# Performance work log

Hardware: AMD Instinct MI355X
Metric: run time of the kernel (lower is better)

Reference implementation:

```python
import jax, jax.numpy as jnp
import numpy as np

SHIFT = 1  # fixed choice for the random +/-1 shift_direction in the torch module


def setup_inputs() -> dict:
    key = jax.random.key(0)
    kx, kw = jax.random.split(key)
    x = jax.random.normal(kx, (128, 128, 56, 56), dtype=jnp.float32)
    W = jax.random.normal(kw, (32, 3, 2, 3, 4), dtype=jnp.float32)
    return {"x": x, "W": W}


def reference(x, W):
    n = x.shape[0]
    # sum-pool over a factor-2 split of the channel dim: (n,128,56,56)->(n,64,56,56)
    t = x.reshape(n, 2, 64, 56, 56).sum(axis=1)
    # view channels as (32 groups, 2): (n,32,2,56,56)
    t = t.reshape(n, 32, 2, 56, 56)
    # first torch unfold == size-3 zero-padded window along the 32-group axis
    tp = jnp.pad(t, ((0, 0), (1, 1), (0, 0), (0, 0), (0, 0)))
    w1 = jnp.stack([tp[:, i:i + 32] for i in range(3)], axis=1)  # (n,3,32,2,56,56)
    # circular shift along the last spatial axis (torch.roll on dim 5)
    w1 = jnp.roll(w1, SHIFT, axis=5)
    # second torch unfold == size-3 zero-padded window along the rolled 56 axis
    wp = jnp.pad(w1, ((0, 0), (0, 0), (0, 0), (0, 0), (0, 0), (1, 1)))
    w2 = jnp.stack([wp[..., l:l + 56] for l in range(3)], axis=5)  # (n,3,32,2,56,3,56)
    # grouped local-conv contraction; axes: n,i=win1(3),j=32,m=2,p=56,l=win2(3),o=56; k=4
    out = jnp.einsum('nijmplo,jimlk->njpok', w2, W)  # (n,32,56,56,4)
    t5 = out.transpose(0, 2, 3, 1, 4).reshape(n, 56, 56, 128)
    t5 = jnp.roll(t5, SHIFT, axis=1)  # roll along first spatial axis
    return t5.transpose(0, 3, 1, 2)  # (n,128,56,56)
```

## Files before the change

### kernel.cpp

```cpp
#include <hip/hip_runtime.h>

#define TPB 512

__device__ __forceinline__ void compute28(const float4* __restrict__ sm4,
                                          const float wt[3][2][3],
                                          int j, int pl, int q0, int qb, int h,
                                          float acc[28]) {
#pragma unroll
    for (int u = 0; u < 28; ++u) acc[u] = 0.f;
#pragma unroll
    for (int i = 0; i < 3; ++i) {
        const int g = j + i - 1;
        if ((unsigned)g < 32u) {
#pragma unroll
            for (int m = 0; m < 2; ++m) {
                const float4* row4 = &sm4[((2 * g + m) * 2 + pl) * 15];
                float fe[32];
                { const float4 t = row4[q0]; fe[0] = t.x; fe[1] = t.y; fe[2] = t.z; fe[3] = t.w; }
#pragma unroll
                for (int q = 1; q < 8; ++q) {
                    const float4 t = row4[qb + q];
                    fe[4 * q + 0] = t.x; fe[4 * q + 1] = t.y;
                    fe[4 * q + 2] = t.z; fe[4 * q + 3] = t.w;
                }
                float va[30];
#pragma unroll
                for (int d = 0; d < 30; ++d) va[d] = fe[d + 2];
                va[0]  = h ? va[0] : 0.f;
                va[29] = h ? 0.f : va[29];
                const float w0 = wt[i][m][0];
                const float w1 = wt[i][m][1];
                const float w2 = wt[i][m][2];
#pragma unroll
                for (int u = 0; u < 28; ++u)
                    acc[u] += w0 * va[u] + w1 * va[u + 1] + w2 * va[u + 2];
            }
        }
    }
}

__device__ __forceinline__ void store2(float4* __restrict__ sm4, float4* __restrict__ o4,
                                       const float acc[28], int tid, int c, int h, int pl,
                                       int n, int p0) {
    const int chalf = c >> 6;
    const int cr = c & 63;
#pragma unroll
    for (int half = 0; half < 2; ++half) {
        __syncthreads();
        if (chalf == half) {
#pragma unroll
            for (int u4 = 0; u4 < 7; ++u4) {
                float4 v4;
                v4.x = acc[4 * u4 + 0];
                v4.y = acc[4 * u4 + 1];
                v4.z = acc[4 * u4 + 2];
                v4.w = acc[4 * u4 + 3];
                sm4[(cr + 64 * pl) * 15 + h * 7 + u4] = v4;
            }
        }
        __syncthreads();
#pragma unroll
        for (int it = 0; it < 4; ++it) {
            const int idx = tid + it * TPB;
            if (idx < 1792) {
                const int chp = idx / 14;
                const int v = idx - chp * 14;
                const int scr = chp & 63;
                const int spl = chp >> 6;
                o4[(size_t)(n * 128 + half * 64 + scr) * 784 + (size_t)(p0 + spl) * 14 + (size_t)v] =
                    sm4[chp * 15 + v];
            }
        }
    }
}

__global__ __launch_bounds__(TPB) void fused_shift_conv(const float* __restrict__ x,
                                                        const float* __restrict__ Wg,
                                                        float* __restrict__ out) {
    const int bid = blockIdx.x;
    const int ptile = bid % 28;
    const int n0 = (bid / 28) * 2;
    const int p0 = ptile * 2;
    const int P0 = (p0 + 55) % 56;
    const int P1 = p0;

    __shared__ float4 sm4[128 * 15];

    const int tid = threadIdx.x;
    const int pl = tid >> 8;
    const int t8 = tid & 255;
    const int h = t8 & 1;
    const int c = t8 >> 1;
    const int j = c >> 2;
    const int k = c & 3;
    const int q0 = h ? 6 : 13;
    const int qb = h ? 6 : -1;

    float wt[3][2][3];
#pragma unroll
    for (int i = 0; i < 3; ++i)
#pragma unroll
        for (int m = 0; m < 2; ++m)
#pragma unroll
            for (int l = 0; l < 3; ++l)
                wt[i][m][l] = Wg[(((j * 3 + i) * 2 + m) * 3 + l) * 4 + k];

    const float4* x4 = reinterpret_cast<const float4*>(x);

#pragma unroll
    for (int it = 0; it < 4; ++it) {
        const int idx = tid + it * TPB;
        if (idx < 1792) {
            const int S = idx / 14;
            const int v = idx - S * 14;
            const int r = S >> 1;
            const int q = S & 1;
            const int Pq = q ? P1 : P0;
            const size_t base = (size_t)(n0 * 128 + r) * 784 + (size_t)Pq * 14 + (size_t)v;
            const float4 a = x4[base];
            const float4 b = x4[base + (size_t)64 * 784];
            float4 s;
            s.x = a.x + b.x; s.y = a.y + b.y; s.z = a.z + b.z; s.w = a.w + b.w;
            sm4[S * 15 + v] = s;
        }
    }

    float4 pa[4], pb[4];
#pragma unroll
    for (int it = 0; it < 4; ++it) {
        const int idx = tid + it * TPB;
        if (idx < 1792) {
            const int S = idx / 14;
            const int v = idx - S * 14;
            const int r = S >> 1;
            const int q = S & 1;
            const int Pq = q ? P1 : P0;
            const size_t base = (size_t)((n0 + 1) * 128 + r) * 784 + (size_t)Pq * 14 + (size_t)v;
            pa[it] = x4[base];
            pb[it] = x4[base + (size_t)64 * 784];
        }
    }

    __syncthreads();

    float acc[28];
    compute28(sm4, wt, j, pl, q0, qb, h, acc);

#pragma unroll
    for (int it = 0; it < 4; ++it) {
        const int idx = tid + it * TPB;
        if (idx < 1792) {
            pa[it].x += pb[it].x; pa[it].y += pb[it].y;
            pa[it].z += pb[it].z; pa[it].w += pb[it].w;
        }
    }

    float4* o4 = reinterpret_cast<float4*>(out);
    store2(sm4, o4, acc, tid, c, h, pl, n0, p0);

    __syncthreads();

#pragma unroll
    for (int it = 0; it < 4; ++it) {
        const int idx = tid + it * TPB;
        if (idx < 1792) {
            const int S = idx / 14;
            const int v = idx - S * 14;
            sm4[S * 15 + v] = pa[it];
        }
    }
    __syncthreads();

    compute28(sm4, wt, j, pl, q0, qb, h, acc);
    store2(sm4, o4, acc, tid, c, h, pl, n0 + 1, p0);
}

extern "C" void kernel_launch(void* const* d_in, const int* in_sizes, int n_in,
                              void* d_out, int out_size, void* d_ws, size_t ws_size,
                              hipStream_t stream) {
    const float* x = (const float*)d_in[0];
    const float* W = (const float*)d_in[1];
    float* out = (float*)d_out;
    const int n = in_sizes[0] / (128 * 56 * 56);
    const int grid = (n / 2) * 28;
    fused_shift_conv<<<grid, TPB, 0, stream>>>(x, W, out);
}
```

Before: 106.7 us.

## Make blocks loop over row tiles with double-buffered LDS prefetch

Each block now handles one image and a quarter of the output rows, iterating over 7 row-pair tiles. The next tile's input is loaded into registers while the current tile computes, then summed into a second LDS buffer. This aims to hide global load latency and cut block launch overhead. The trade-off is fewer blocks (n*4) and doubled shared memory, which can reduce occupancy and parallelism.

```diff
diff --git a/kernel.cpp b/kernel.cpp
--- a/kernel.cpp
+++ b/kernel.cpp
@@ -1,6 +1,7 @@
 #include <hip/hip_runtime.h>
 
 #define TPB 512
+#define PT  7
 
 __device__ __forceinline__ void compute28(const float4* __restrict__ sm4,
                                           const float wt[3][2][3],
@@ -78,13 +79,12 @@
                                                         const float* __restrict__ Wg,
                                                         float* __restrict__ out) {
     const int bid = blockIdx.x;
-    const int ptile = bid % 28;
-    const int n0 = (bid / 28) * 2;
-    const int p0 = ptile * 2;
-    const int P0 = (p0 + 55) % 56;
-    const int P1 = p0;
-
-    __shared__ float4 sm4[128 * 15];
+    const int quarter = bid & 3;
+    const int n = bid >> 2;
+    const int pt0 = quarter * PT;
+
+    __shared__ float4 smA[128 * 15];
+    __shared__ float4 smB[128 * 15];
 
     const int tid = threadIdx.x;
     const int pl = tid >> 8;
@@ -96,6 +96,9 @@
     const int q0 = h ? 6 : 13;
     const int qb = h ? 6 : -1;
 
+    const int sidx = tid < 448 ? -1 : 0;
+    (void)sidx;
+
     float wt[3][2][3];
 #pragma unroll
     for (int i = 0; i < 3; ++i)
@@ -106,73 +109,86 @@
                 wt[i][m][l] = Wg[(((j * 3 + i) * 2 + m) * 3 + l) * 4 + k];
 
     const float4* x4 = reinterpret_cast<const float4*>(x);
-
-#pragma unroll
-    for (int it = 0; it < 4; ++it) {
-        const int idx = tid + it * TPB;
-        if (idx < 1792) {
-            const int S = idx / 14;
-            const int v = idx - S * 14;
-            const int r = S >> 1;
-            const int q = S & 1;
-            const int Pq = q ? P1 : P0;
-            const size_t base = (size_t)(n0 * 128 + r) * 784 + (size_t)Pq * 14 + (size_t)v;
-            const float4 a = x4[base];
-            const float4 b = x4[base + (size_t)64 * 784];
-            float4 s;
-            s.x = a.x + b.x; s.y = a.y + b.y; s.z = a.z + b.z; s.w = a.w + b.w;
-            sm4[S * 15 + v] = s;
-        }
-    }
-
-    float4 pa[4], pb[4];
-#pragma unroll
-    for (int it = 0; it < 4; ++it) {
-        const int idx = tid + it * TPB;
-        if (idx < 1792) {
-            const int S = idx / 14;
-            const int v = idx - S * 14;
-            const int r = S >> 1;
-            const int q = S & 1;
-            const int Pq = q ? P1 : P0;
-            const size_t base = (size_t)((n0 + 1) * 128 + r) * 784 + (size_t)Pq * 14 + (size_t)v;
-            pa[it] = x4[base];
-            pb[it] = x4[base + (size_t)64 * 784];
-        }
-    }
-
-    __syncthreads();
-
-    float acc[28];
-    compute28(sm4, wt, j, pl, q0, qb, h, acc);
-
-#pragma unroll
-    for (int it = 0; it < 4; ++it) {
-        const int idx = tid + it * TPB;
-        if (idx < 1792) {
-            pa[it].x += pb[it].x; pa[it].y += pb[it].y;
-            pa[it].z += pb[it].z; pa[it].w += pb[it].w;
-        }
-    }
-
     float4* o4 = reinterpret_cast<float4*>(out);
-    store2(sm4, o4, acc, tid, c, h, pl, n0, p0);
-
-    __syncthreads();
-
-#pragma unroll
-    for (int it = 0; it < 4; ++it) {
-        const int idx = tid + it * TPB;
-        if (idx < 1792) {
-            const int S = idx / 14;
-            const int v = idx - S * 14;
-            sm4[S * 15 + v] = pa[it];
-        }
-    }
-    __syncthreads();
-
-    compute28(sm4, wt, j, pl, q0, qb, h, acc);
-    store2(sm4, o4, acc, tid, c, h, pl, n0 + 1, p0);
+
+    {
+        const int p0 = (pt0) * 2;
+        const int P0 = (p0 + 55) % 56;
+        const int P1 = p0;
+#pragma unroll
+        for (int it = 0; it < 4; ++it) {
+            const int idx = tid + it * TPB;
+            if (idx < 1792) {
+                const int S = idx / 14;
+                const int v = idx - S * 14;
+                const int r = S >> 1;
+                const int q = S & 1;
+                const int Pq = q ? P1 : P0;
+                const size_t base = (size_t)(n * 128 + r) * 784 + (size_t)Pq * 14 + (size_t)v;
+                const float4 a = x4[base];
+                const float4 b = x4[base + (size_t)64 * 784];
+                float4 s;
+                s.x = a.x + b.x; s.y = a.y + b.y; s.z = a.z + b.z; s.w = a.w + b.w;
+                smA[S * 15 + v] = s;
+            }
+        }
+    }
+
+    float4* bcur = smA;
+    float4* bnxt = smB;
+
+#pragma unroll 1
+    for (int t = 0; t < PT; ++t) {
+        const int p0 = (pt0 + t) * 2;
+
+        float4 pa[4], pb[4];
+        const bool more = (t + 1 < PT);
+        if (more) {
+            const int p0n = (pt0 + t + 1) * 2;
+            const int P0n = (p0n + 55) % 56;
+            const int P1n = p0n;
+#pragma unroll
+            for (int it = 0; it < 4; ++it) {
+                const int idx = tid + it * TPB;
+                if (idx < 1792) {
+                    const int S = idx / 14;
+                    const int v = idx - S * 14;
+                    const int r = S >> 1;
+                    const int q = S & 1;
+                    const int Pq = q ? P1n : P0n;
+                    const size_t base = (size_t)(n * 128 + r) * 784 + (size_t)Pq * 14 + (size_t)v;
+                    pa[it] = x4[base];
+                    pb[it] = x4[base + (size_t)64 * 784];
+                }
+            }
+        }
+
+        __syncthreads();
+
+        float acc[28];
+        compute28(bcur, wt, j, pl, q0, qb, h, acc);
+
+        store2(bcur, o4, acc, tid, c, h, pl, n, p0);
+
+        if (more) {
+#pragma unroll
+            for (int it = 0; it < 4; ++it) {
+                const int idx = tid + it * TPB;
+                if (idx < 1792) {
+                    const int S = idx / 14;
+                    const int v = idx - S * 14;
+                    float4 s;
+                    s.x = pa[it].x + pb[it].x;
+                    s.y = pa[it].y + pb[it].y;
+                    s.z = pa[it].z + pb[it].z;
+                    s.w = pa[it].w + pb[it].w;
+                    bnxt[S * 15 + v] = s;
+                }
+            }
+        }
+
+        float4* tmp = bcur; bcur = bnxt; bnxt = tmp;
+    }
 }
 
 extern "C" void kernel_launch(void* const* d_in, const int* in_sizes, int n_in,
@@ -182,6 +198,6 @@
     const float* W = (const float*)d_in[1];
     float* out = (float*)d_out;
     const int n = in_sizes[0] / (128 * 56 * 56);
-    const int grid = (n / 2) * 28;
+    const int grid = n * 4;
     fused_shift_conv<<<grid, TPB, 0, stream>>>(x, W, out);
 }
```

New measurement: 101.4 us. -5.0%, faster.
